# Kernel optimization log

Measured on AMD Instinct MI355X. Metric: run time of the kernel, lower is better.

The kernel has to match this reference:

```python
import jax, jax.numpy as jnp
import numpy as np

N = 50000          # nodes
E = 400000         # edges
MUL = 32           # multiplicity per irrep
NUM_NEIGHBORS = 8.0
INV_SQRT3 = 1.0 / np.sqrt(3.0)  # w3j(1,1,0) coefficient


def setup_inputs() -> dict:
    key = jax.random.key(0)
    ks = jax.random.split(key, 20)
    inp = {
        # node_input: 32x0e (dim 32) + 32x1o (dim 96) = 128
        "node_input": jax.random.normal(ks[0], (N, 4 * MUL), jnp.float32),
        "node_attr": jnp.ones((N, 1), jnp.float32),           # 1x0e trivial attr
        "edge_src": jax.random.randint(ks[1], (E,), 0, N, jnp.int32),
        "edge_dst": jax.random.randint(ks[2], (E,), 0, N, jnp.int32),
        "edge_attr": jax.random.normal(ks[3], (E, 4), jnp.float32),   # 1x0e + 1x1o
        "edge_scalars": jax.random.normal(ks[4], (E, 16), jnp.float32),
        # FullyConnectedTensorProduct weights (uvw, node_attr has mul 1)
        "w_sc0": jax.random.normal(ks[5], (MUL, MUL), jnp.float32),
        "w_sc1": jax.random.normal(ks[6], (MUL, MUL), jnp.float32),
        "w_lin1_0": jax.random.normal(ks[7], (MUL, MUL), jnp.float32),
        "w_lin1_1": jax.random.normal(ks[8], (MUL, MUL), jnp.float32),
        # radial FC net -> per-edge TP weights (numel = 4*MUL = 128)
        "fc_w1": jax.random.normal(ks[9], (16, 64), jnp.float32),
        "fc_w2": jax.random.normal(ks[10], (64, 4 * MUL), jnp.float32),
        # lin2: irreps_mid (64x0e+64x1o) x attr -> output
        "w_lin2_0": jax.random.normal(ks[11], (2 * MUL, MUL), jnp.float32),
        "w_lin2_1": jax.random.normal(ks[12], (2 * MUL, MUL), jnp.float32),
        # alpha: irreps_mid x attr -> 0e (zero-init in original; small randn for a nontrivial test)
        "w_alpha": 0.1 * jax.random.normal(ks[13], (2 * MUL, 1), jnp.float32),
        # sc_edges: irreps_mid x edge_attr -> edge_attr
        "w_se0a": jax.random.normal(ks[14], (2 * MUL,), jnp.float32),  # mid0e x ea0e -> 0e
        "w_se0b": jax.random.normal(ks[15], (2 * MUL,), jnp.float32),  # mid1o x ea1o -> 0e
        "w_se1a": jax.random.normal(ks[16], (2 * MUL,), jnp.float32),  # mid0e x ea1o -> 1o
        "w_se1b": jax.random.normal(ks[17], (2 * MUL,), jnp.float32),  # mid1o x ea0e -> 1o
    }
    return inp


def reference(node_input, node_attr, edge_src, edge_dst, edge_attr, edge_scalars,
              w_sc0, w_sc1, w_lin1_0, w_lin1_1, fc_w1, fc_w2,
              w_lin2_0, w_lin2_1, w_alpha, w_se0a, w_se0b, w_se1a, w_se1b):
    inv_nn = 1.0 / jnp.sqrt(jnp.asarray(NUM_NEIGHBORS, node_input.dtype))
    n = node_input.shape[0]
    x0 = node_input[:, :MUL]                       # (N, 32)   32x0e
    x1 = node_input[:, MUL:].reshape(n, MUL, 3)    # (N, 32, 3) 32x1o
    a = node_attr                                  # (N, 1)
    s_in = 1.0 / np.sqrt(MUL)                      # FCTP fan-in normalization

    # self-connection: FCTP(input, attr) -> output
    sc0 = (x0 @ w_sc0) * a * s_in
    sc1 = jnp.einsum('num,uw->nwm', x1, w_sc1) * a[:, :, None] * s_in
    node_self = jnp.concatenate([sc0, sc1.reshape(n, 3 * MUL)], axis=1)  # (N, 128)

    # lin1: FCTP(input, attr) -> input irreps
    f0 = (x0 @ w_lin1_0) * a * s_in
    f1 = jnp.einsum('num,uw->nwm', x1, w_lin1_1) * a[:, :, None] * s_in

    # gather source node features per edge
    g0 = f0[edge_src]                              # (E, 32)
    g1 = f1[edge_src]                              # (E, 32, 3)
    ea0 = edge_attr[:, :1]                         # (E, 1)   1x0e
    ea1 = edge_attr[:, 1:]                         # (E, 3)   1x1o

    # radial net -> per-edge TP weights (FullyConnectedNet with sin activation)
    h = jnp.sin(edge_scalars @ fc_w1 * (1.0 / np.sqrt(16.0)))
    w = h @ fc_w2 * (1.0 / np.sqrt(64.0))          # (E, 128)
    wA, wB, wC, wD = jnp.split(w, 4, axis=1)       # each (E, 32)

    # uvu tensor product, 4 instructions
    mA = wA * g0 * ea0                                           # 0e x 0e -> 0e
    mD = wD * jnp.einsum('eum,em->eu', g1, ea1) * INV_SQRT3      # 1o x 1o -> 0e
    mB = (wB * g0)[:, :, None] * ea1[:, None, :]                 # 0e x 1o -> 1o
    mC = (wC[:, :, None] * g1) * ea0[:, :, None]                 # 1o x 0e -> 1o
    mid0 = jnp.concatenate([mA, mD], axis=1)       # (E, 64)  64x0e
    mid1 = jnp.concatenate([mB, mC], axis=1)       # (E, 64, 3) 64x1o

    # scatter-add to destination nodes
    n0 = jax.ops.segment_sum(mid0, edge_dst, num_segments=n) * inv_nn
    n1 = jax.ops.segment_sum(mid1, edge_dst, num_segments=n) * inv_nn

    s_mid = 1.0 / np.sqrt(2 * MUL)
    out0 = (n0 @ w_lin2_0) * a * s_mid
    out1 = jnp.einsum('num,uw->nwm', n1, w_lin2_1) * a[:, :, None] * s_mid
    node_conv = jnp.concatenate([out0, out1.reshape(n, 3 * MUL)], axis=1)

    # alpha gate (sc.output_mask is all ones here, so alpha = 1 - 1 + alpha*1)
    alpha = (n0 @ w_alpha) * a * s_mid             # (N, 1)
    node_conv_out = node_self + alpha * node_conv  # (N, 128)

    # sc_edges: FCTP(mid, edge_attr) -> edge_attr irreps; fan-in = 128 per output
    s_se = 1.0 / np.sqrt(4 * MUL)
    se0 = ((mid0 @ w_se0a) * ea0[:, 0]
           + jnp.einsum('eum,em,u->e', mid1, ea1, w_se0b) * INV_SQRT3) * s_se
    se1 = ((mid0 @ w_se1a)[:, None] * ea1
           + jnp.einsum('eum,u->em', mid1, w_se1b) * ea0) * s_se
    edge_conv_out = edge_attr + jnp.concatenate([se0[:, None], se1], axis=1) * inv_nn

    return node_conv_out, edge_conv_out
```

## Files before the change

kernel.cpp:

```cpp
#include <hip/hip_runtime.h>
#include <math.h>

#define N_NODES 50000
#define E_EDGES 400000
#define NPRE_BLOCKS 6250
#define NHIST_BLOCKS 1563
#define NEDGE_BLOCKS 6250

typedef _Float16 f16x2 __attribute__((ext_vector_type(2)));
typedef _Float16 f16x4 __attribute__((ext_vector_type(4)));
typedef _Float16 f16x8 __attribute__((ext_vector_type(8)));
typedef float    f32x4 __attribute__((ext_vector_type(4)));

static constexpr float S_IN      = 0.17677669529663687f;
static constexpr float S_MID     = 0.125f;
static constexpr float S_SE      = 0.08838834764831843f;
static constexpr float INV_NN    = 0.35355339059327373f;
static constexpr float INV_SQRT3 = 0.5773502691896258f;
static constexpr float FC1_S     = 0.25f;
static constexpr float FC2_S     = 0.125f;

#define WAVE_LDS_FENCE() asm volatile("s_waitcnt lgkmcnt(0)" ::: "memory")

__device__ inline float wave_reduce_dpp(float v) {
    int x;
    x = __builtin_amdgcn_update_dpp(0, __float_as_int(v), 0x111, 0xf, 0xf, true); v += __int_as_float(x);
    x = __builtin_amdgcn_update_dpp(0, __float_as_int(v), 0x112, 0xf, 0xf, true); v += __int_as_float(x);
    x = __builtin_amdgcn_update_dpp(0, __float_as_int(v), 0x114, 0xf, 0xf, true); v += __int_as_float(x);
    x = __builtin_amdgcn_update_dpp(0, __float_as_int(v), 0x118, 0xf, 0xf, true); v += __int_as_float(x);
    x = __builtin_amdgcn_update_dpp(0, __float_as_int(v), 0x142, 0xa, 0xf, true); v += __int_as_float(x);
    x = __builtin_amdgcn_update_dpp(0, __float_as_int(v), 0x143, 0xc, 0xf, true); v += __int_as_float(x);
    return __int_as_float(__builtin_amdgcn_readlane(__float_as_int(v), 63));
}

__global__ __launch_bounds__(256) void pre_hist_kernel(
    const float* __restrict__ node_input, const float* __restrict__ node_attr,
    const float* __restrict__ w_sc0, const float* __restrict__ w_sc1,
    const float* __restrict__ w_lin1_0, const float* __restrict__ w_lin1_1,
    float* __restrict__ out_self, _Float16* __restrict__ ws_h,
    const int* __restrict__ edge_dst, int* __restrict__ counts,
    const float* __restrict__ edge_scalars, _Float16* __restrict__ ES_h,
    float* __restrict__ nacc)
{
    const int t = threadIdx.x;
    if (blockIdx.x >= NPRE_BLOCKS) {
        const int e = (blockIdx.x - NPRE_BLOCKS) * 256 + t;
        if (e < E_EDGES) {
            atomicAdd(&counts[edge_dst[e]], 1);
            const float4* s4 = (const float4*)edge_scalars + (size_t)e * 4;
            _Float16* dp = ES_h + (size_t)e * 16;
            #pragma unroll
            for (int i = 0; i < 4; ++i) {
                const float4 v = s4[i];
                f16x4 p = {(_Float16)v.x, (_Float16)v.y, (_Float16)v.z, (_Float16)v.w};
                *(f16x4*)&dp[i * 4] = p;
            }
        }
        return;
    }
    const int n0 = blockIdx.x * 8;
    __shared__ __align__(16) float sx[8 * 128];
    __shared__ float sa[8];
    {
        const int k = t >> 5, q = t & 31;
        const float4 v = ((const float4*)(node_input + (size_t)n0 * 128))[t];
        if (q < 8) {
            *(float4*)&sx[k * 128 + q * 4] = v;
        } else {
            const int base = q * 4 - 32;
            const float vv[4] = {v.x, v.y, v.z, v.w};
            #pragma unroll
            for (int j = 0; j < 4; ++j) {
                const int uj = (base + j) / 3, mj = (base + j) % 3;
                sx[k * 128 + 32 + mj * 32 + uj] = vv[j];
            }
        }
    }
    {
        float4* nz = (float4*)(nacc + (size_t)n0 * 256);
        const float4 z4 = {0.f, 0.f, 0.f, 0.f};
        nz[t] = z4; nz[t + 256] = z4;
    }
    if (t < 8) sa[t] = node_attr[n0 + t];
    __syncthreads();

    const int half = t >> 7;
    const int idx  = t & 127;
    float wcol[32];
    int xoff = 0;
    if (idx < 32) {
        const float* __restrict__ W = half ? w_lin1_0 : w_sc0;
        #pragma unroll
        for (int u = 0; u < 32; ++u) wcol[u] = W[u * 32 + idx];
    } else {
        const float* __restrict__ W = half ? w_lin1_1 : w_sc1;
        const int j = idx - 32;
        const int w = j / 3; const int m = j % 3;
        xoff = 32 + m * 32;
        #pragma unroll
        for (int u = 0; u < 32; ++u) wcol[u] = W[u * 32 + w];
    }
    #pragma unroll
    for (int k = 0; k < 8; ++k) {
        const float* xb = sx + k * 128 + xoff;
        float acc = 0.f;
        #pragma unroll
        for (int u4 = 0; u4 < 8; ++u4) {
            const f32x4 xv = *(const f32x4*)&xb[u4 * 4];
            acc += xv[0] * wcol[u4 * 4 + 0];
            acc += xv[1] * wcol[u4 * 4 + 1];
            acc += xv[2] * wcol[u4 * 4 + 2];
            acc += xv[3] * wcol[u4 * 4 + 3];
        }
        const float v = acc * sa[k] * S_IN;
        if (half) ws_h[(size_t)(n0 + k) * 128 + idx] = (_Float16)v;
        else      out_self[(size_t)(n0 + k) * 128 + idx] = v;
    }
}

__global__ __launch_bounds__(1024) void scan_block_kernel(
    const int* __restrict__ counts, int* __restrict__ cursor, int* __restrict__ bsum,
    const float* __restrict__ fc_w1, const float* __restrict__ fc_w2,
    const float* __restrict__ w_se0a, const float* __restrict__ w_se0b,
    const float* __restrict__ w_se1a, const float* __restrict__ w_se1b,
    _Float16* __restrict__ W2T_g, _Float16* __restrict__ W1T_g,
    _Float16* __restrict__ BT_g)
{
    const int t = threadIdx.x;
    if (blockIdx.x == 49) {
        for (int u = t; u < 8192; u += 1024) {
            const int k = u >> 7, c = u & 127;
            W2T_g[c * 72 + k] = (_Float16)fc_w2[u];
        }
        {
            W2T_g[(t >> 3) * 72 + 64 + (t & 7)] = (_Float16)0.f;
        }
        {
            const int j = t >> 4, k = t & 15;
            W1T_g[t] = (_Float16)fc_w1[k * 64 + j];
        }
        for (int u = t; u < 2112; u += 1024) BT_g[u] = (_Float16)0.f;
        __syncthreads();
        if (t < 256) {
            const int uu = t & 63, p = t >> 6;
            const float ev = (p == 0) ? w_se0a[uu] : w_se1b[uu];
            const float ov = (p == 0) ? w_se1a[uu] : w_se0b[uu];
            BT_g[(2 * p) * 264 + 4 * uu + p]     = (_Float16)ev;
            BT_g[(2 * p + 1) * 264 + 4 * uu + p] = (_Float16)ov;
        }
        return;
    }
    const int idx = blockIdx.x * 1024 + t;
    const int c   = (idx < N_NODES) ? counts[idx] : 0;
    int v = c, x;
    x = __builtin_amdgcn_update_dpp(0, v, 0x111, 0xf, 0xf, true); v += x;
    x = __builtin_amdgcn_update_dpp(0, v, 0x112, 0xf, 0xf, true); v += x;
    x = __builtin_amdgcn_update_dpp(0, v, 0x114, 0xf, 0xf, true); v += x;
    x = __builtin_amdgcn_update_dpp(0, v, 0x118, 0xf, 0xf, true); v += x;
    x = __builtin_amdgcn_update_dpp(0, v, 0x142, 0xa, 0xf, true); v += x;
    x = __builtin_amdgcn_update_dpp(0, v, 0x143, 0xc, 0xf, true); v += x;
    __shared__ int swv[16], sex[16];
    const int wid = t >> 6;
    if ((t & 63) == 63) swv[wid] = v;
    __syncthreads();
    if (t < 16) {
        int a = 0;
        for (int j = 0; j < t; ++j) a += swv[j];
        sex[t] = a;
        if (t == 15) bsum[blockIdx.x] = a + swv[15];
    }
    __syncthreads();
    if (idx < N_NODES) cursor[idx] = v - c + sex[wid];
}

__global__ __launch_bounds__(1024) void scan_fixup_kernel(
    int* __restrict__ cursor, const int* __restrict__ bsum)
{
    __shared__ int boff_s;
    const int t = threadIdx.x;
    if (t < 64) {
        int v = (t < (int)blockIdx.x) ? bsum[t] : 0;
        #pragma unroll
        for (int off = 32; off >= 1; off >>= 1) v += __shfl_down(v, off, 64);
        if (t == 0) boff_s = v;
    }
    __syncthreads();
    const int idx = blockIdx.x * 1024 + t;
    if (idx < N_NODES) cursor[idx] += boff_s;
}

__global__ __launch_bounds__(256) void scatter_kernel(
    const int* __restrict__ edge_dst, int* __restrict__ cursor,
    int* __restrict__ sorted_eid)
{
    const int e = blockIdx.x * 256 + threadIdx.x;
    if (e < E_EDGES) {
        const int p = atomicAdd(&cursor[edge_dst[e]], 1);
        sorted_eid[p] = e;
    }
}

__global__ __launch_bounds__(256, 4) void edge_kernel(
    const _Float16* __restrict__ ws_h,
    const int* __restrict__ edge_src, const int* __restrict__ edge_dst,
    const float* __restrict__ edge_attr, const _Float16* __restrict__ ES_h,
    const _Float16* __restrict__ W2T_g, const _Float16* __restrict__ W1T_g,
    const _Float16* __restrict__ BT_g,
    const int* __restrict__ sorted_eid,
    float* __restrict__ nacc, float* __restrict__ edge_out)
{
    __shared__ __align__(16) _Float16 sArena[17536];
    __shared__ __align__(16) float sEA[64 * 4];
    __shared__ __align__(16) float sDep[4][36];
    __shared__ int sSRC[64];
    __shared__ int sDST[64];
    __shared__ int sEID[64];

    _Float16* __restrict__ sHT   = sArena;
    _Float16* __restrict__ sWt   = sArena + 4608;
    _Float16* __restrict__ sMidA = sArena + 13312;

    const int t    = threadIdx.x;
    const int lane = t & 63;
    const int wv   = t >> 6;
    const int quad = lane >> 4;
    const int mm   = lane & 15;

    const int orig = blockIdx.x;
    const int xcd  = orig & 7;
    constexpr int q = NEDGE_BLOCKS >> 3, r = NEDGE_BLOCKS & 7;
    const int bid = (xcd < r ? xcd * (q + 1) : r * (q + 1) + (xcd - r) * q) + (orig >> 3);
    const int e0 = bid * 64;
    const int eb = wv * 16;

    f16x8 a_w1[4];
    f16x8 b_es = {};
    if (quad < 2) {
        const int myeid = sorted_eid[e0 + eb + mm];
        b_es = *(const f16x8*)&ES_h[((unsigned)myeid << 4) + quad * 8];
        #pragma unroll
        for (int jt = 0; jt < 4; ++jt)
            a_w1[jt] = *(const f16x8*)&W1T_g[(jt * 16 + mm) * 16 + quad * 8];
    } else {
        #pragma unroll
        for (int jt = 0; jt < 4; ++jt) a_w1[jt] = (f16x8){};
    }
    f16x8 bt[8];
    #pragma unroll
    for (int ks = 0; ks < 8; ++ks)
        bt[ks] = *(const f16x8*)&BT_g[(mm & 7) * 264 + ks * 32 + quad * 8];

    if (lane < 16) {
        const int eid = sorted_eid[e0 + eb + lane];
        sEID[eb + lane] = eid;
        sSRC[eb + lane] = edge_src[eid];
        sDST[eb + lane] = edge_dst[eid];
        *(float4*)&sEA[(eb + lane) * 4] = ((const float4*)edge_attr)[eid];
    }
    WAVE_LDS_FENCE();

    const bool hi = lane >= 32;
    const int  u  = lane - 32;
    const int idxA = hi ? (32 + 3 * u) : lane;
    const int idxB = hi ? (33 + 3 * u) : lane;
    const int idxC = hi ? (34 + 3 * u) : lane;
    const int col1 = hi ? (96 + u) : lane;
    const int col2 = hi ? (64 + u) : (32 + lane);

    float ga[4][4], gb[4][4], gc[4][4];
    #pragma unroll
    for (int b = 0; b < 4; ++b)
        #pragma unroll
        for (int i = 0; i < 4; ++i) {
            const unsigned off = (unsigned)sSRC[eb + b * 4 + i] << 7;
            ga[b][i] = (float)ws_h[off + idxA];
            gb[b][i] = (float)ws_h[off + idxB];
            gc[b][i] = (float)ws_h[off + idxC];
        }
    asm volatile("" ::: "memory");

    #pragma unroll
    for (int jt = 0; jt < 4; ++jt) {
        f32x4 d = {0.f, 0.f, 0.f, 0.f};
        d = __builtin_amdgcn_mfma_f32_16x16x32_f16(a_w1[jt], b_es, d, 0, 0, 0);
        f16x4 hv;
        hv[0] = (_Float16)__sinf(d[0] * FC1_S);
        hv[1] = (_Float16)__sinf(d[1] * FC1_S);
        hv[2] = (_Float16)__sinf(d[2] * FC1_S);
        hv[3] = (_Float16)__sinf(d[3] * FC1_S);
        *(f16x4*)&sHT[(eb + mm) * 72 + jt * 16 + quad * 4] = hv;
    }
    WAVE_LDS_FENCE();

    f32x4 dacc[8];
    {
        const f16x8 b_lo = *(const f16x8*)&sHT[(eb + mm) * 72 + quad * 8];
        const f16x8 b_hi = *(const f16x8*)&sHT[(eb + mm) * 72 + 32 + quad * 8];
        #pragma unroll
        for (int ct = 0; ct < 8; ++ct) {
            const f16x8 a_lo = *(const f16x8*)&W2T_g[(ct * 16 + mm) * 72 + quad * 8];
            const f16x8 a_hi = *(const f16x8*)&W2T_g[(ct * 16 + mm) * 72 + 32 + quad * 8];
            f32x4 d = {0.f, 0.f, 0.f, 0.f};
            d = __builtin_amdgcn_mfma_f32_16x16x32_f16(a_lo, b_lo, d, 0, 0, 0);
            d = __builtin_amdgcn_mfma_f32_16x16x32_f16(a_hi, b_hi, d, 0, 0, 0);
            dacc[ct] = d;
        }
    }

    #pragma unroll
    for (int ct = 0; ct < 8; ++ct) {
        f16x4 v;
        v[0] = (_Float16)(dacc[ct][0] * FC2_S);
        v[1] = (_Float16)(dacc[ct][1] * FC2_S);
        v[2] = (_Float16)(dacc[ct][2] * FC2_S);
        v[3] = (_Float16)(dacc[ct][3] * FC2_S);
        *(f16x4*)&sWt[(eb + mm) * 136 + ct * 16 + quad * 4] = v;
    }
    WAVE_LDS_FENCE();

    int   cur = -1;
    float am0 = 0.f, axx = 0.f, ayy = 0.f, azz = 0.f;
    _Float16* __restrict__ myA = sMidA + wv * 1056;
    const _Float16* __restrict__ arow = myA + (mm & 3) * 264;

    #pragma unroll
    for (int b = 0; b < 4; ++b) {
        float w1b[4], w2b[4];
        #pragma unroll
        for (int i = 0; i < 4; ++i) {
            w1b[i] = (float)sWt[(eb + b * 4 + i) * 136 + col1];
            w2b[i] = (float)sWt[(eb + b * 4 + i) * 136 + col2];
        }
        #pragma unroll
        for (int i = 0; i < 4; ++i) {
            const int el  = eb + b * 4 + i;
            const int dst = sDST[el];
            const float ea0 = sEA[el * 4 + 0];
            const float e1x = sEA[el * 4 + 1];
            const float e1y = sEA[el * 4 + 2];
            const float e1z = sEA[el * 4 + 3];
            const float w1v = w1b[i];
            const float w2v = w2b[i];

            float mid0, m1x, m1y, m1z;
            if (!hi) {
                mid0 = w1v * ga[b][i] * ea0;
                const float wbg = w2v * ga[b][i];
                m1x = wbg * e1x; m1y = wbg * e1y; m1z = wbg * e1z;
            } else {
                const float dot = ga[b][i] * e1x + gb[b][i] * e1y + gc[b][i] * e1z;
                mid0 = w1v * dot * INV_SQRT3;
                const float wce = w2v * ea0;
                m1x = wce * ga[b][i]; m1y = wce * gb[b][i]; m1z = wce * gc[b][i];
            }

            if (dst != cur) {
                if (cur >= 0) {
                    float* np_ = nacc + ((unsigned)cur << 8);
                    atomicAdd(np_ + lane, am0);
                    atomicAdd(np_ + 64 + lane, axx);
                    atomicAdd(np_ + 128 + lane, ayy);
                    atomicAdd(np_ + 192 + lane, azz);
                }
                cur = dst; am0 = axx = ayy = azz = 0.f;
            }
            am0 += mid0; axx += m1x; ayy += m1y; azz += m1z;

            f16x4 mv;
            mv[0] = (_Float16)mid0; mv[1] = (_Float16)m1x;
            mv[2] = (_Float16)m1y;  mv[3] = (_Float16)m1z;
            *(f16x4*)&myA[i * 264 + 4 * lane] = mv;
        }

        f32x4 d = {0.f, 0.f, 0.f, 0.f};
        #pragma unroll
        for (int ks = 0; ks < 8; ++ks) {
            const f16x8 a = *(const f16x8*)&arow[ks * 32 + quad * 8];
            d = __builtin_amdgcn_mfma_f32_16x16x32_f16(a, bt[ks], d, 0, 0, 0);
        }
        if (lane < 8) {
            float4 f4; f4.x = d[0]; f4.y = d[1]; f4.z = d[2]; f4.w = d[3];
            *(float4*)&sDep[wv][lane * 4] = f4;
        }
        if (lane < 4) {
            const int el = eb + b * 4 + lane;
            const float c0 = sDep[wv][ 0 + lane], c1 = sDep[wv][ 4 + lane];
            const float c2 = sDep[wv][ 8 + lane], c3 = sDep[wv][12 + lane];
            const float c4 = sDep[wv][16 + lane], c5 = sDep[wv][20 + lane];
            const float c6 = sDep[wv][24 + lane], c7 = sDep[wv][28 + lane];
            const float ea0 = sEA[el * 4 + 0];
            const float e1x = sEA[el * 4 + 1];
            const float e1y = sEA[el * 4 + 2];
            const float e1z = sEA[el * 4 + 3];
            const float s0 = c0 * ea0 + (c3 * e1x + c5 * e1y + c7 * e1z) * INV_SQRT3;
            float4 o;
            o.x = ea0 + s0 * S_SE * INV_NN;
            o.y = e1x + (c1 * e1x + c2 * ea0) * S_SE * INV_NN;
            o.z = e1y + (c1 * e1y + c4 * ea0) * S_SE * INV_NN;
            o.w = e1z + (c1 * e1z + c6 * ea0) * S_SE * INV_NN;
            *(float4*)&edge_out[(unsigned)sEID[el] << 2] = o;
        }
    }
    if (cur >= 0) {
        float* np_ = nacc + ((unsigned)cur << 8);
        atomicAdd(np_ + lane, am0);
        atomicAdd(np_ + 64 + lane, axx);
        atomicAdd(np_ + 128 + lane, ayy);
        atomicAdd(np_ + 192 + lane, azz);
    }
}

__global__ __launch_bounds__(128) void node_post_kernel(
    const float* __restrict__ nacc, const float* __restrict__ node_attr,
    const float* __restrict__ w_lin2_0, const float* __restrict__ w_lin2_1,
    const float* __restrict__ w_alpha, float* __restrict__ out)
{
    const int n0 = blockIdx.x * 8, t = threadIdx.x;
    __shared__ __align__(16) float sn[8 * 256];
    __shared__ float salpha[8];
    const float4* src = (const float4*)(nacc + (size_t)n0 * 256);
    #pragma unroll
    for (int i = 0; i < 4; ++i) ((float4*)sn)[t + i * 128] = src[t + i * 128];
    __syncthreads();

    if (t < 64) {
        const float wa = w_alpha[t];
        #pragma unroll
        for (int k = 0; k < 8; ++k) {
            const float r = wave_reduce_dpp(sn[k * 256 + t] * wa);
            if (t == 0) salpha[k] = r;
        }
    }
    __syncthreads();

    float wcol[64];
    int xoff = 0;
    if (t < 32) {
        #pragma unroll
        for (int u = 0; u < 64; ++u) wcol[u] = w_lin2_0[u * 32 + t];
    } else {
        const int j = t - 32; const int w = j / 3; const int m = j % 3;
        xoff = 64 + m * 64;
        #pragma unroll
        for (int u = 0; u < 64; ++u) wcol[u] = w_lin2_1[u * 32 + w];
    }
    #pragma unroll
    for (int k = 0; k < 8; ++k) {
        const float* xb = sn + k * 256 + xoff;
        float acc = 0.f;
        #pragma unroll
        for (int u4 = 0; u4 < 16; ++u4) {
            const f32x4 xv = *(const f32x4*)&xb[u4 * 4];
            acc += xv[0] * wcol[u4 * 4 + 0];
            acc += xv[1] * wcol[u4 * 4 + 1];
            acc += xv[2] * wcol[u4 * 4 + 2];
            acc += xv[3] * wcol[u4 * 4 + 3];
        }
        const float a  = node_attr[n0 + k];
        const float sc = a * S_MID * INV_NN;
        const size_t o = (size_t)(n0 + k) * 128 + t;
        out[o] = out[o] + (salpha[k] * sc) * (acc * sc);
    }
}

extern "C" void kernel_launch(void* const* d_in, const int* in_sizes, int n_in,
                              void* d_out, int out_size, void* d_ws, size_t ws_size,
                              hipStream_t stream)
{
    const float* node_input   = (const float*)d_in[0];
    const float* node_attr    = (const float*)d_in[1];
    const int*   edge_src     = (const int*)d_in[2];
    const int*   edge_dst     = (const int*)d_in[3];
    const float* edge_attr    = (const float*)d_in[4];
    const float* edge_scalars = (const float*)d_in[5];
    const float* w_sc0        = (const float*)d_in[6];
    const float* w_sc1        = (const float*)d_in[7];
    const float* w_lin1_0     = (const float*)d_in[8];
    const float* w_lin1_1     = (const float*)d_in[9];
    const float* fc_w1        = (const float*)d_in[10];
    const float* fc_w2        = (const float*)d_in[11];
    const float* w_lin2_0     = (const float*)d_in[12];
    const float* w_lin2_1     = (const float*)d_in[13];
    const float* w_alpha      = (const float*)d_in[14];
    const float* w_se0a       = (const float*)d_in[15];
    const float* w_se0b       = (const float*)d_in[16];
    const float* w_se1a       = (const float*)d_in[17];
    const float* w_se1b       = (const float*)d_in[18];

    float* out      = (float*)d_out;
    float* edge_out = out + (size_t)N_NODES * 128;

    _Float16* ws_h = (_Float16*)d_ws;
    _Float16* ES_h = ws_h + (size_t)N_NODES * 128;
    float* nacc   = (float*)((char*)d_ws + (size_t)N_NODES * 128 * 4);
    int*   counts = (int*)(nacc + (size_t)N_NODES * 256);
    int*   cursor = counts + N_NODES;
    int*   sid    = cursor + N_NODES;
    int*   bsum   = sid + E_EDGES;
    _Float16* W2T_g = (_Float16*)(bsum + 64);
    _Float16* W1T_g = W2T_g + 9216;
    _Float16* BT_g  = W1T_g + 1024;

    hipMemsetAsync(counts, 0, N_NODES * sizeof(int), stream);

    pre_hist_kernel<<<NPRE_BLOCKS + NHIST_BLOCKS, 256, 0, stream>>>(
        node_input, node_attr, w_sc0, w_sc1, w_lin1_0, w_lin1_1, out, ws_h,
        edge_dst, counts, edge_scalars, ES_h, nacc);

    scan_block_kernel<<<50, 1024, 0, stream>>>(counts, cursor, bsum,
        fc_w1, fc_w2, w_se0a, w_se0b, w_se1a, w_se1b, W2T_g, W1T_g, BT_g);
    scan_fixup_kernel<<<49, 1024, 0, stream>>>(cursor, bsum);
    scatter_kernel<<<(E_EDGES + 255) / 256, 256, 0, stream>>>(edge_dst, cursor, sid);

    edge_kernel<<<NEDGE_BLOCKS, 256, 0, stream>>>(
        ws_h, edge_src, edge_dst, edge_attr, ES_h, W2T_g, W1T_g, BT_g,
        sid, nacc, edge_out);

    node_post_kernel<<<N_NODES / 8, 128, 0, stream>>>(
        nacc, node_attr, w_lin2_0, w_lin2_1, w_alpha, out);
}
```

Baseline: 358.1 us.

## Fuse scan kernels with grid sync and move self-connection into node post

Merges the block scan and fixup kernels into one launch that uses an atomic-counter grid barrier, removing one kernel launch. It also moves the self-connection linear (w_sc0/w_sc1) from the pre-pass into the node post kernel. The post kernel then writes the output once instead of the pre-pass writing out_self and the post kernel reading it back and updating it, which saves a full read-modify-write of the node output. The grid barrier relies on all 50 blocks being co-resident, and node_input is now read a second time in the post kernel.

```diff
diff --git a/kernel.cpp b/kernel.cpp
--- a/kernel.cpp
+++ b/kernel.cpp
@@ -6,6 +6,7 @@
 #define NPRE_BLOCKS 6250
 #define NHIST_BLOCKS 1563
 #define NEDGE_BLOCKS 6250
+#define NSCAN_BLOCKS 50
 
 typedef _Float16 f16x2 __attribute__((ext_vector_type(2)));
 typedef _Float16 f16x4 __attribute__((ext_vector_type(4)));
@@ -33,16 +34,27 @@
     return __int_as_float(__builtin_amdgcn_readlane(__float_as_int(v), 63));
 }
 
+__device__ inline void gsync(int* cnt, int target) {
+    __syncthreads();
+    if (threadIdx.x == 0) {
+        __hip_atomic_fetch_add(cnt, 1, __ATOMIC_ACQ_REL, __HIP_MEMORY_SCOPE_AGENT);
+        while (__hip_atomic_load(cnt, __ATOMIC_ACQUIRE, __HIP_MEMORY_SCOPE_AGENT) < target)
+            __builtin_amdgcn_s_sleep(8);
+    }
+    __syncthreads();
+    __threadfence();
+}
+
 __global__ __launch_bounds__(256) void pre_hist_kernel(
     const float* __restrict__ node_input, const float* __restrict__ node_attr,
-    const float* __restrict__ w_sc0, const float* __restrict__ w_sc1,
     const float* __restrict__ w_lin1_0, const float* __restrict__ w_lin1_1,
-    float* __restrict__ out_self, _Float16* __restrict__ ws_h,
+    _Float16* __restrict__ ws_h,
     const int* __restrict__ edge_dst, int* __restrict__ counts,
     const float* __restrict__ edge_scalars, _Float16* __restrict__ ES_h,
-    float* __restrict__ nacc)
+    float* __restrict__ nacc, int* __restrict__ sync_cnt)
 {
     const int t = threadIdx.x;
+    if (blockIdx.x == 0 && t == 0) *sync_cnt = 0;
     if (blockIdx.x >= NPRE_BLOCKS) {
         const int e = (blockIdx.x - NPRE_BLOCKS) * 256 + t;
         if (e < E_EDGES) {
@@ -84,25 +96,24 @@
     if (t < 8) sa[t] = node_attr[n0 + t];
     __syncthreads();
 
-    const int half = t >> 7;
-    const int idx  = t & 127;
+    const int col   = t & 127;
+    const int kbase = (t >> 7) * 4;
     float wcol[32];
     int xoff = 0;
-    if (idx < 32) {
-        const float* __restrict__ W = half ? w_lin1_0 : w_sc0;
-        #pragma unroll
-        for (int u = 0; u < 32; ++u) wcol[u] = W[u * 32 + idx];
+    if (col < 32) {
+        #pragma unroll
+        for (int u = 0; u < 32; ++u) wcol[u] = w_lin1_0[u * 32 + col];
     } else {
-        const float* __restrict__ W = half ? w_lin1_1 : w_sc1;
-        const int j = idx - 32;
+        const int j = col - 32;
         const int w = j / 3; const int m = j % 3;
         xoff = 32 + m * 32;
         #pragma unroll
-        for (int u = 0; u < 32; ++u) wcol[u] = W[u * 32 + w];
-    }
-    #pragma unroll
-    for (int k = 0; k < 8; ++k) {
-        const float* xb = sx + k * 128 + xoff;
+        for (int u = 0; u < 32; ++u) wcol[u] = w_lin1_1[u * 32 + w];
+    }
+    #pragma unroll
+    for (int k = 0; k < 4; ++k) {
+        const int kk = kbase + k;
+        const float* xb = sx + kk * 128 + xoff;
         float acc = 0.f;
         #pragma unroll
         for (int u4 = 0; u4 < 8; ++u4) {
@@ -112,22 +123,46 @@
             acc += xv[2] * wcol[u4 * 4 + 2];
             acc += xv[3] * wcol[u4 * 4 + 3];
         }
-        const float v = acc * sa[k] * S_IN;
-        if (half) ws_h[(size_t)(n0 + k) * 128 + idx] = (_Float16)v;
-        else      out_self[(size_t)(n0 + k) * 128 + idx] = v;
-    }
-}
-
-__global__ __launch_bounds__(1024) void scan_block_kernel(
-    const int* __restrict__ counts, int* __restrict__ cursor, int* __restrict__ bsum,
+        ws_h[(size_t)(n0 + kk) * 128 + col] = (_Float16)(acc * sa[kk] * S_IN);
+    }
+}
+
+__global__ __launch_bounds__(1024) void scan_fused_kernel(
+    const int* __restrict__ counts, int* __restrict__ cursor,
+    int* __restrict__ bsum, int* __restrict__ sync_cnt,
     const float* __restrict__ fc_w1, const float* __restrict__ fc_w2,
     const float* __restrict__ w_se0a, const float* __restrict__ w_se0b,
     const float* __restrict__ w_se1a, const float* __restrict__ w_se1b,
     _Float16* __restrict__ W2T_g, _Float16* __restrict__ W1T_g,
     _Float16* __restrict__ BT_g)
 {
-    const int t = threadIdx.x;
-    if (blockIdx.x == 49) {
+    const int t = threadIdx.x, b = blockIdx.x;
+    const int idx = b * 1024 + t;
+    __shared__ int swv[16], sex[16];
+    __shared__ int boff_s;
+    int myexc = 0;
+
+    if (b < 49) {
+        const int c = (idx < N_NODES) ? counts[idx] : 0;
+        int v = c, x;
+        x = __builtin_amdgcn_update_dpp(0, v, 0x111, 0xf, 0xf, true); v += x;
+        x = __builtin_amdgcn_update_dpp(0, v, 0x112, 0xf, 0xf, true); v += x;
+        x = __builtin_amdgcn_update_dpp(0, v, 0x114, 0xf, 0xf, true); v += x;
+        x = __builtin_amdgcn_update_dpp(0, v, 0x118, 0xf, 0xf, true); v += x;
+        x = __builtin_amdgcn_update_dpp(0, v, 0x142, 0xa, 0xf, true); v += x;
+        x = __builtin_amdgcn_update_dpp(0, v, 0x143, 0xc, 0xf, true); v += x;
+        const int wid = t >> 6;
+        if ((t & 63) == 63) swv[wid] = v;
+        __syncthreads();
+        if (t < 16) {
+            int a = 0;
+            for (int j = 0; j < t; ++j) a += swv[j];
+            sex[t] = a;
+            if (t == 15) bsum[b] = a + swv[15];
+        }
+        __syncthreads();
+        myexc = v - c + sex[wid];
+    } else {
         for (int u = t; u < 8192; u += 1024) {
             const int k = u >> 7, c = u & 127;
             W2T_g[c * 72 + k] = (_Float16)fc_w2[u];
@@ -148,45 +183,19 @@
             BT_g[(2 * p) * 264 + 4 * uu + p]     = (_Float16)ev;
             BT_g[(2 * p + 1) * 264 + 4 * uu + p] = (_Float16)ov;
         }
-        return;
-    }
-    const int idx = blockIdx.x * 1024 + t;
-    const int c   = (idx < N_NODES) ? counts[idx] : 0;
-    int v = c, x;
-    x = __builtin_amdgcn_update_dpp(0, v, 0x111, 0xf, 0xf, true); v += x;
-    x = __builtin_amdgcn_update_dpp(0, v, 0x112, 0xf, 0xf, true); v += x;
-    x = __builtin_amdgcn_update_dpp(0, v, 0x114, 0xf, 0xf, true); v += x;
-    x = __builtin_amdgcn_update_dpp(0, v, 0x118, 0xf, 0xf, true); v += x;
-    x = __builtin_amdgcn_update_dpp(0, v, 0x142, 0xa, 0xf, true); v += x;
-    x = __builtin_amdgcn_update_dpp(0, v, 0x143, 0xc, 0xf, true); v += x;
-    __shared__ int swv[16], sex[16];
-    const int wid = t >> 6;
-    if ((t & 63) == 63) swv[wid] = v;
-    __syncthreads();
-    if (t < 16) {
-        int a = 0;
-        for (int j = 0; j < t; ++j) a += swv[j];
-        sex[t] = a;
-        if (t == 15) bsum[blockIdx.x] = a + swv[15];
-    }
-    __syncthreads();
-    if (idx < N_NODES) cursor[idx] = v - c + sex[wid];
-}
-
-__global__ __launch_bounds__(1024) void scan_fixup_kernel(
-    int* __restrict__ cursor, const int* __restrict__ bsum)
-{
-    __shared__ int boff_s;
-    const int t = threadIdx.x;
-    if (t < 64) {
-        int v = (t < (int)blockIdx.x) ? bsum[t] : 0;
-        #pragma unroll
-        for (int off = 32; off >= 1; off >>= 1) v += __shfl_down(v, off, 64);
-        if (t == 0) boff_s = v;
-    }
-    __syncthreads();
-    const int idx = blockIdx.x * 1024 + t;
-    if (idx < N_NODES) cursor[idx] += boff_s;
+    }
+    gsync(sync_cnt, NSCAN_BLOCKS);
+
+    if (b < 49) {
+        if (t < 64) {
+            int vv = (t < b) ? bsum[t] : 0;
+            #pragma unroll
+            for (int off = 32; off >= 1; off >>= 1) vv += __shfl_down(vv, off, 64);
+            if (t == 0) boff_s = vv;
+        }
+        __syncthreads();
+        if (idx < N_NODES) cursor[idx] = myexc + boff_s;
+    }
 }
 
 __global__ __launch_bounds__(256) void scatter_kernel(
@@ -411,16 +420,36 @@
 }
 
 __global__ __launch_bounds__(128) void node_post_kernel(
-    const float* __restrict__ nacc, const float* __restrict__ node_attr,
+    const float* __restrict__ nacc, const float* __restrict__ node_input,
+    const float* __restrict__ node_attr,
+    const float* __restrict__ w_sc0, const float* __restrict__ w_sc1,
     const float* __restrict__ w_lin2_0, const float* __restrict__ w_lin2_1,
     const float* __restrict__ w_alpha, float* __restrict__ out)
 {
     const int n0 = blockIdx.x * 8, t = threadIdx.x;
     __shared__ __align__(16) float sn[8 * 256];
+    __shared__ __align__(16) float sx[8 * 128];
     __shared__ float salpha[8];
     const float4* src = (const float4*)(nacc + (size_t)n0 * 256);
     #pragma unroll
     for (int i = 0; i < 4; ++i) ((float4*)sn)[t + i * 128] = src[t + i * 128];
+    #pragma unroll
+    for (int i = 0; i < 2; ++i) {
+        const int uu = t + i * 128;
+        const int k = uu >> 5, qq = uu & 31;
+        const float4 v = ((const float4*)(node_input + (size_t)n0 * 128))[uu];
+        if (qq < 8) {
+            *(float4*)&sx[k * 128 + qq * 4] = v;
+        } else {
+            const int base = qq * 4 - 32;
+            const float vv[4] = {v.x, v.y, v.z, v.w};
+            #pragma unroll
+            for (int j = 0; j < 4; ++j) {
+                const int uj = (base + j) / 3, mj = (base + j) % 3;
+                sx[k * 128 + 32 + mj * 32 + uj] = vv[j];
+            }
+        }
+    }
     __syncthreads();
 
     if (t < 64) {
@@ -434,15 +463,21 @@
     __syncthreads();
 
     float wcol[64];
-    int xoff = 0;
+    float wsc[32];
+    int xoff = 0, sxoff = 0;
     if (t < 32) {
         #pragma unroll
         for (int u = 0; u < 64; ++u) wcol[u] = w_lin2_0[u * 32 + t];
+        #pragma unroll
+        for (int u = 0; u < 32; ++u) wsc[u] = w_sc0[u * 32 + t];
     } else {
         const int j = t - 32; const int w = j / 3; const int m = j % 3;
-        xoff = 64 + m * 64;
+        xoff  = 64 + m * 64;
+        sxoff = 32 + m * 32;
         #pragma unroll
         for (int u = 0; u < 64; ++u) wcol[u] = w_lin2_1[u * 32 + w];
+        #pragma unroll
+        for (int u = 0; u < 32; ++u) wsc[u] = w_sc1[u * 32 + w];
     }
     #pragma unroll
     for (int k = 0; k < 8; ++k) {
@@ -456,10 +491,20 @@
             acc += xv[2] * wcol[u4 * 4 + 2];
             acc += xv[3] * wcol[u4 * 4 + 3];
         }
+        const float* xb2 = sx + k * 128 + sxoff;
+        float sacc = 0.f;
+        #pragma unroll
+        for (int u4 = 0; u4 < 8; ++u4) {
+            const f32x4 xv = *(const f32x4*)&xb2[u4 * 4];
+            sacc += xv[0] * wsc[u4 * 4 + 0];
+            sacc += xv[1] * wsc[u4 * 4 + 1];
+            sacc += xv[2] * wsc[u4 * 4 + 2];
+            sacc += xv[3] * wsc[u4 * 4 + 3];
+        }
         const float a  = node_attr[n0 + k];
         const float sc = a * S_MID * INV_NN;
         const size_t o = (size_t)(n0 + k) * 128 + t;
-        out[o] = out[o] + (salpha[k] * sc) * (acc * sc);
+        out[o] = sacc * a * S_IN + (salpha[k] * sc) * (acc * sc);
     }
 }
 
@@ -500,16 +545,18 @@
     _Float16* W2T_g = (_Float16*)(bsum + 64);
     _Float16* W1T_g = W2T_g + 9216;
     _Float16* BT_g  = W1T_g + 1024;
+    int* sync_cnt   = (int*)(BT_g + 2112);
 
     hipMemsetAsync(counts, 0, N_NODES * sizeof(int), stream);
 
     pre_hist_kernel<<<NPRE_BLOCKS + NHIST_BLOCKS, 256, 0, stream>>>(
-        node_input, node_attr, w_sc0, w_sc1, w_lin1_0, w_lin1_1, out, ws_h,
-        edge_dst, counts, edge_scalars, ES_h, nacc);
-
-    scan_block_kernel<<<50, 1024, 0, stream>>>(counts, cursor, bsum,
+        node_input, node_attr, w_lin1_0, w_lin1_1, ws_h,
+        edge_dst, counts, edge_scalars, ES_h, nacc, sync_cnt);
+
+    scan_fused_kernel<<<NSCAN_BLOCKS, 1024, 0, stream>>>(
+        counts, cursor, bsum, sync_cnt,
         fc_w1, fc_w2, w_se0a, w_se0b, w_se1a, w_se1b, W2T_g, W1T_g, BT_g);
-    scan_fixup_kernel<<<49, 1024, 0, stream>>>(cursor, bsum);
+
     scatter_kernel<<<(E_EDGES + 255) / 256, 256, 0, stream>>>(edge_dst, cursor, sid);
 
     edge_kernel<<<NEDGE_BLOCKS, 256, 0, stream>>>(
@@ -517,5 +564,6 @@
         sid, nacc, edge_out);
 
     node_post_kernel<<<N_NODES / 8, 128, 0, stream>>>(
-        nacc, node_attr, w_lin2_0, w_lin2_1, w_alpha, out);
-}
+        nacc, node_input, node_attr, w_sc0, w_sc1, w_lin2_0, w_lin2_1,
+        w_alpha, out);
+}
```

New measurement: 384.9 us. 1.07x slower.

## Fuse scan fixup into scan kernel via grid barrier; convert edge scalars in-kernel

Applied to the files above, without the earlier changes.

Merges the block scan and fixup kernels into one launch that uses an atomic-counter grid barrier across the 50 co-resident blocks, removing one kernel launch. It also drops the precomputed fp16 copy of edge_scalars: the edge kernel now reads the fp32 scalars directly through the sorted edge ids and converts them in registers, which removes a write and re-read pass. The cost is a spin-wait barrier that relies on all blocks being resident at once, and gathered fp32 loads that are twice as wide as the old fp16 ones.

```diff
diff --git a/kernel.cpp b/kernel.cpp
--- a/kernel.cpp
+++ b/kernel.cpp
@@ -6,6 +6,7 @@
 #define NPRE_BLOCKS 6250
 #define NHIST_BLOCKS 1563
 #define NEDGE_BLOCKS 6250
+#define NSCAN_BLOCKS 50
 
 typedef _Float16 f16x2 __attribute__((ext_vector_type(2)));
 typedef _Float16 f16x4 __attribute__((ext_vector_type(4)));
@@ -33,29 +34,30 @@
     return __int_as_float(__builtin_amdgcn_readlane(__float_as_int(v), 63));
 }
 
+__device__ inline void gsync(int* cnt, int target) {
+    __syncthreads();
+    if (threadIdx.x == 0) {
+        __hip_atomic_fetch_add(cnt, 1, __ATOMIC_ACQ_REL, __HIP_MEMORY_SCOPE_AGENT);
+        while (__hip_atomic_load(cnt, __ATOMIC_ACQUIRE, __HIP_MEMORY_SCOPE_AGENT) < target)
+            __builtin_amdgcn_s_sleep(8);
+    }
+    __syncthreads();
+    __threadfence();
+}
+
 __global__ __launch_bounds__(256) void pre_hist_kernel(
     const float* __restrict__ node_input, const float* __restrict__ node_attr,
     const float* __restrict__ w_sc0, const float* __restrict__ w_sc1,
     const float* __restrict__ w_lin1_0, const float* __restrict__ w_lin1_1,
     float* __restrict__ out_self, _Float16* __restrict__ ws_h,
     const int* __restrict__ edge_dst, int* __restrict__ counts,
-    const float* __restrict__ edge_scalars, _Float16* __restrict__ ES_h,
-    float* __restrict__ nacc)
+    float* __restrict__ nacc, int* __restrict__ sync_cnt)
 {
     const int t = threadIdx.x;
+    if (blockIdx.x == 0 && t == 0) *sync_cnt = 0;
     if (blockIdx.x >= NPRE_BLOCKS) {
         const int e = (blockIdx.x - NPRE_BLOCKS) * 256 + t;
-        if (e < E_EDGES) {
-            atomicAdd(&counts[edge_dst[e]], 1);
-            const float4* s4 = (const float4*)edge_scalars + (size_t)e * 4;
-            _Float16* dp = ES_h + (size_t)e * 16;
-            #pragma unroll
-            for (int i = 0; i < 4; ++i) {
-                const float4 v = s4[i];
-                f16x4 p = {(_Float16)v.x, (_Float16)v.y, (_Float16)v.z, (_Float16)v.w};
-                *(f16x4*)&dp[i * 4] = p;
-            }
-        }
+        if (e < E_EDGES) atomicAdd(&counts[edge_dst[e]], 1);
         return;
     }
     const int n0 = blockIdx.x * 8;
@@ -118,16 +120,42 @@
     }
 }
 
-__global__ __launch_bounds__(1024) void scan_block_kernel(
-    const int* __restrict__ counts, int* __restrict__ cursor, int* __restrict__ bsum,
+__global__ __launch_bounds__(1024) void scan_fused_kernel(
+    const int* __restrict__ counts, int* __restrict__ cursor,
+    int* __restrict__ bsum, int* __restrict__ sync_cnt,
     const float* __restrict__ fc_w1, const float* __restrict__ fc_w2,
     const float* __restrict__ w_se0a, const float* __restrict__ w_se0b,
     const float* __restrict__ w_se1a, const float* __restrict__ w_se1b,
     _Float16* __restrict__ W2T_g, _Float16* __restrict__ W1T_g,
     _Float16* __restrict__ BT_g)
 {
-    const int t = threadIdx.x;
-    if (blockIdx.x == 49) {
+    const int t = threadIdx.x, b = blockIdx.x;
+    const int idx = b * 1024 + t;
+    __shared__ int swv[16], sex[16];
+    __shared__ int boff_s;
+    int myexc = 0;
+
+    if (b < 49) {
+        const int c = (idx < N_NODES) ? counts[idx] : 0;
+        int v = c, x;
+        x = __builtin_amdgcn_update_dpp(0, v, 0x111, 0xf, 0xf, true); v += x;
+        x = __builtin_amdgcn_update_dpp(0, v, 0x112, 0xf, 0xf, true); v += x;
+        x = __builtin_amdgcn_update_dpp(0, v, 0x114, 0xf, 0xf, true); v += x;
+        x = __builtin_amdgcn_update_dpp(0, v, 0x118, 0xf, 0xf, true); v += x;
+        x = __builtin_amdgcn_update_dpp(0, v, 0x142, 0xa, 0xf, true); v += x;
+        x = __builtin_amdgcn_update_dpp(0, v, 0x143, 0xc, 0xf, true); v += x;
+        const int wid = t >> 6;
+        if ((t & 63) == 63) swv[wid] = v;
+        __syncthreads();
+        if (t < 16) {
+            int a = 0;
+            for (int j = 0; j < t; ++j) a += swv[j];
+            sex[t] = a;
+            if (t == 15) bsum[b] = a + swv[15];
+        }
+        __syncthreads();
+        myexc = v - c + sex[wid];
+    } else {
         for (int u = t; u < 8192; u += 1024) {
             const int k = u >> 7, c = u & 127;
             W2T_g[c * 72 + k] = (_Float16)fc_w2[u];
@@ -148,45 +176,19 @@
             BT_g[(2 * p) * 264 + 4 * uu + p]     = (_Float16)ev;
             BT_g[(2 * p + 1) * 264 + 4 * uu + p] = (_Float16)ov;
         }
-        return;
-    }
-    const int idx = blockIdx.x * 1024 + t;
-    const int c   = (idx < N_NODES) ? counts[idx] : 0;
-    int v = c, x;
-    x = __builtin_amdgcn_update_dpp(0, v, 0x111, 0xf, 0xf, true); v += x;
-    x = __builtin_amdgcn_update_dpp(0, v, 0x112, 0xf, 0xf, true); v += x;
-    x = __builtin_amdgcn_update_dpp(0, v, 0x114, 0xf, 0xf, true); v += x;
-    x = __builtin_amdgcn_update_dpp(0, v, 0x118, 0xf, 0xf, true); v += x;
-    x = __builtin_amdgcn_update_dpp(0, v, 0x142, 0xa, 0xf, true); v += x;
-    x = __builtin_amdgcn_update_dpp(0, v, 0x143, 0xc, 0xf, true); v += x;
-    __shared__ int swv[16], sex[16];
-    const int wid = t >> 6;
-    if ((t & 63) == 63) swv[wid] = v;
-    __syncthreads();
-    if (t < 16) {
-        int a = 0;
-        for (int j = 0; j < t; ++j) a += swv[j];
-        sex[t] = a;
-        if (t == 15) bsum[blockIdx.x] = a + swv[15];
-    }
-    __syncthreads();
-    if (idx < N_NODES) cursor[idx] = v - c + sex[wid];
-}
-
-__global__ __launch_bounds__(1024) void scan_fixup_kernel(
-    int* __restrict__ cursor, const int* __restrict__ bsum)
-{
-    __shared__ int boff_s;
-    const int t = threadIdx.x;
-    if (t < 64) {
-        int v = (t < (int)blockIdx.x) ? bsum[t] : 0;
-        #pragma unroll
-        for (int off = 32; off >= 1; off >>= 1) v += __shfl_down(v, off, 64);
-        if (t == 0) boff_s = v;
-    }
-    __syncthreads();
-    const int idx = blockIdx.x * 1024 + t;
-    if (idx < N_NODES) cursor[idx] += boff_s;
+    }
+    gsync(sync_cnt, NSCAN_BLOCKS);
+
+    if (b < 49) {
+        if (t < 64) {
+            int vv = (t < b) ? bsum[t] : 0;
+            #pragma unroll
+            for (int off = 32; off >= 1; off >>= 1) vv += __shfl_down(vv, off, 64);
+            if (t == 0) boff_s = vv;
+        }
+        __syncthreads();
+        if (idx < N_NODES) cursor[idx] = myexc + boff_s;
+    }
 }
 
 __global__ __launch_bounds__(256) void scatter_kernel(
@@ -203,7 +205,7 @@
 __global__ __launch_bounds__(256, 4) void edge_kernel(
     const _Float16* __restrict__ ws_h,
     const int* __restrict__ edge_src, const int* __restrict__ edge_dst,
-    const float* __restrict__ edge_attr, const _Float16* __restrict__ ES_h,
+    const float* __restrict__ edge_attr, const float* __restrict__ edge_scalars,
     const _Float16* __restrict__ W2T_g, const _Float16* __restrict__ W1T_g,
     const _Float16* __restrict__ BT_g,
     const int* __restrict__ sorted_eid,
@@ -237,7 +239,13 @@
     f16x8 b_es = {};
     if (quad < 2) {
         const int myeid = sorted_eid[e0 + eb + mm];
-        b_es = *(const f16x8*)&ES_h[((unsigned)myeid << 4) + quad * 8];
+        const f32x4* esp = (const f32x4*)edge_scalars + ((unsigned)myeid << 2) + (quad << 1);
+        const f32x4 v0 = esp[0];
+        const f32x4 v1 = esp[1];
+        b_es[0] = (_Float16)v0[0]; b_es[1] = (_Float16)v0[1];
+        b_es[2] = (_Float16)v0[2]; b_es[3] = (_Float16)v0[3];
+        b_es[4] = (_Float16)v1[0]; b_es[5] = (_Float16)v1[1];
+        b_es[6] = (_Float16)v1[2]; b_es[7] = (_Float16)v1[3];
         #pragma unroll
         for (int jt = 0; jt < 4; ++jt)
             a_w1[jt] = *(const f16x8*)&W1T_g[(jt * 16 + mm) * 16 + quad * 8];
@@ -491,7 +499,6 @@
     float* edge_out = out + (size_t)N_NODES * 128;
 
     _Float16* ws_h = (_Float16*)d_ws;
-    _Float16* ES_h = ws_h + (size_t)N_NODES * 128;
     float* nacc   = (float*)((char*)d_ws + (size_t)N_NODES * 128 * 4);
     int*   counts = (int*)(nacc + (size_t)N_NODES * 256);
     int*   cursor = counts + N_NODES;
@@ -500,20 +507,22 @@
     _Float16* W2T_g = (_Float16*)(bsum + 64);
     _Float16* W1T_g = W2T_g + 9216;
     _Float16* BT_g  = W1T_g + 1024;
+    int* sync_cnt   = (int*)(BT_g + 2112);
 
     hipMemsetAsync(counts, 0, N_NODES * sizeof(int), stream);
 
     pre_hist_kernel<<<NPRE_BLOCKS + NHIST_BLOCKS, 256, 0, stream>>>(
         node_input, node_attr, w_sc0, w_sc1, w_lin1_0, w_lin1_1, out, ws_h,
-        edge_dst, counts, edge_scalars, ES_h, nacc);
-
-    scan_block_kernel<<<50, 1024, 0, stream>>>(counts, cursor, bsum,
+        edge_dst, counts, nacc, sync_cnt);
+
+    scan_fused_kernel<<<NSCAN_BLOCKS, 1024, 0, stream>>>(
+        counts, cursor, bsum, sync_cnt,
         fc_w1, fc_w2, w_se0a, w_se0b, w_se1a, w_se1b, W2T_g, W1T_g, BT_g);
-    scan_fixup_kernel<<<49, 1024, 0, stream>>>(cursor, bsum);
+
     scatter_kernel<<<(E_EDGES + 255) / 256, 256, 0, stream>>>(edge_dst, cursor, sid);
 
     edge_kernel<<<NEDGE_BLOCKS, 256, 0, stream>>>(
-        ws_h, edge_src, edge_dst, edge_attr, ES_h, W2T_g, W1T_g, BT_g,
+        ws_h, edge_src, edge_dst, edge_attr, edge_scalars, W2T_g, W1T_g, BT_g,
         sid, nacc, edge_out);
 
     node_post_kernel<<<N_NODES / 8, 128, 0, stream>>>(
```

Result: slower. 387.7 us (+8.3%).
